# Performance work log

Measured on AMD Instinct MI355X. Metric: run time of the kernel, lower is better.

Reference implementation:

```python
import jax, jax.numpy as jnp
import numpy as np
import math

# Zero-indexed Fano plane lines: {i, i+1, i+3} mod 7
FANO_LINES = np.array([[0,1,3],[1,2,4],[2,3,5],[3,4,6],[4,5,0],[5,6,1],[6,0,2]])
WINDOW = 16  # local window hardcoded in create_expanded_mask

HIDDEN = 896
HEADS = 7
HEAD_DIM = HIDDEN // HEADS  # 128
B, T = 4, 2048


def fano_expanded_mask(T, causal):
    # line membership per head: [7, T] -> True where (j % 7) in line
    jm = np.arange(T) % 7
    line_hit = np.zeros((7, T), dtype=bool)
    for h in range(7):
        line_hit[h] = np.isin(jm, FANO_LINES[h])
    line_hit = jnp.asarray(line_hit)
    i = jnp.arange(T)[:, None]
    j = jnp.arange(T)[None, :]
    if causal:
        causal_m = j <= i                      # [T, T]
        local = (j >= i - WINDOW) & (j <= i)   # causal local window [i-16, i]
        mask = (line_hit[:, None, :] & causal_m[None]) | local[None]
    else:
        local = (j >= i - WINDOW) & (j <= i + WINDOW)
        mask = line_hit[:, None, :] | local[None]
    return mask  # [7, T, T], True = attend


def setup_inputs() -> dict:
    key = jax.random.key(0)
    kx, kq, kk, kv, ko = jax.random.split(key, 5)
    s = 1.0 / math.sqrt(HIDDEN)
    return {
        "x": jax.random.normal(kx, (B, T, HIDDEN), dtype=jnp.float32),
        "Wq": jax.random.normal(kq, (HEADS, HIDDEN, HEAD_DIM), dtype=jnp.float32) * s,
        "Wk": jax.random.normal(kk, (HEADS, HIDDEN, HEAD_DIM), dtype=jnp.float32) * s,
        "Wv": jax.random.normal(kv, (HEADS, HIDDEN, HEAD_DIM), dtype=jnp.float32) * s,
        "Wo": jax.random.normal(ko, (HIDDEN, HIDDEN), dtype=jnp.float32) * s,
        "is_causal": 1,
    }


def reference(x, Wq, Wk, Wv, Wo, is_causal):
    Bx, Tx, H = x.shape
    d = Wq.shape[-1]
    scale = 1.0 / math.sqrt(d)
    # per-head projections (no bias): [7, B, T, d]
    q = jnp.einsum('bth,nhd->nbtd', x, Wq)
    k = jnp.einsum('bth,nhd->nbtd', x, Wk)
    v = jnp.einsum('bth,nhd->nbtd', x, Wv)
    mask = fano_expanded_mask(Tx, bool(is_causal))        # [7, T, T]
    attn = jnp.einsum('nbtd,nbsd->nbts', q, k) * scale    # [7, B, T, T]
    attn = jnp.where(mask[:, None], attn, -jnp.inf)
    attn = jax.nn.softmax(attn, axis=-1)                  # every row has j=i valid
    out = jnp.einsum('nbts,nbsd->nbtd', attn, v)          # [7, B, T, d]
    combined = out.transpose(1, 2, 0, 3).reshape(Bx, Tx, H)  # concat heads
    return combined @ Wo.T
```

## Files before the change

### kernel.cpp

```cpp
#include <hip/hip_runtime.h>
#include <hip/hip_bf16.h>

#define HIDDEN 896
#define HEADS 7
#define HDIM 128
#define BB 4
#define TT 2048
#define MTOT (BB*TT)

#define KSP 132
#define VSP 68
#define PSP 68

#define SCP 896

typedef short bf16x8 __attribute__((ext_vector_type(8)));
typedef float f32x4 __attribute__((ext_vector_type(4)));

__device__ __forceinline__ short f2bf(float f) {
    union { float f; unsigned u; } v; v.f = f;
    unsigned r = (v.u + 0x7FFF + ((v.u >> 16) & 1)) >> 16;
    return (short)r;
}

__device__ __forceinline__ void gll16(const short* g, short* l) {
    __builtin_amdgcn_global_load_lds(
        (const __attribute__((address_space(1))) unsigned int*)g,
        (__attribute__((address_space(3))) unsigned int*)l, 16, 0, 0);
}

__device__ __forceinline__ unsigned linemask(int h) {
    return ((0x0Bu << h) | (0x0Bu >> (7 - h))) & 0x7Fu;
}
__device__ __forceinline__ int linecnt(unsigned m, int X) {
    return (X / 7) * 3 + __popc(m & ((1u << (X % 7)) - 1u));
}

#define NB_CASTX (MTOT * HIDDEN / 1024)
#define NB_CASTWO (HIDDEN * HIDDEN / 1024)
#define NB_TRANS (28 * 4 * 21)
__global__ __launch_bounds__(256) void prep_fused(
    const float* __restrict__ x, const float* __restrict__ Wo,
    const float* __restrict__ Wq, const float* __restrict__ Wk,
    const float* __restrict__ Wv,
    short* __restrict__ xb, short* __restrict__ Wob, short* __restrict__ Wt)
{
    __shared__ float tile[32][33];
    const int bid = blockIdx.x;
    if (bid < NB_CASTX) {
        int base = (bid * 256 + threadIdx.x) * 4;
        float4 v = *(const float4*)(x + base);
        short4 o;
        o.x = f2bf(v.x); o.y = f2bf(v.y); o.z = f2bf(v.z); o.w = f2bf(v.w);
        *(short4*)(xb + base) = o;
    } else if (bid < NB_CASTX + NB_CASTWO) {
        int base = ((bid - NB_CASTX) * 256 + threadIdx.x) * 4;
        float4 v = *(const float4*)(Wo + base);
        short4 o;
        o.x = f2bf(v.x); o.y = f2bf(v.y); o.z = f2bf(v.z); o.w = f2bf(v.w);
        *(short4*)(Wob + base) = o;
    } else {
        int t = bid - NB_CASTX - NB_CASTWO;
        const int z = t / 112;
        const int rem = t % 112;
        const int bx = rem % 28, by = rem / 28;
        const int type = z / 7, head = z % 7;
        const float* src = (type == 0 ? Wq : (type == 1 ? Wk : Wv)) + head * (HIDDEN * HDIM);
        short* dst = Wt + (size_t)z * (HDIM * HIDDEN);
        const int r0 = bx * 32, c0 = by * 32;
        const int tx = threadIdx.x & 31, ty = threadIdx.x >> 5;
        for (int i = 0; i < 4; i++)
            tile[ty * 4 + i][tx] = src[(r0 + ty * 4 + i) * HDIM + c0 + tx];
        __syncthreads();
        for (int i = 0; i < 4; i++)
            dst[(c0 + ty * 4 + i) * HIDDEN + r0 + tx] = f2bf(tile[tx][ty * 4 + i]);
    }
}

__global__ __launch_bounds__(256) void qkv_gemm(
    const short* __restrict__ xb, const short* __restrict__ Wt,
    short* __restrict__ Q, short* __restrict__ Kk, short* __restrict__ Vt)
{
    __shared__ short Ash[3 * 128 * 32];
    __shared__ short Bsh[3 * 128 * 32];
    const int orig = blockIdx.x;
    const int sblk = (orig & 7) * 168 + (orig >> 3);
    const int z = sblk % 21;
    const int m0 = (sblk / 21) * 128;
    const int head = z % 7, type = z / 7;
    const short* Wz = Wt + (size_t)z * (HDIM * HIDDEN);

    const int tid = threadIdx.x;
    const int wave = tid >> 6, lane = tid & 63;
    const int quad = lane >> 4, l16 = lane & 15;
    const int wm = (wave >> 1) * 64, wn = (wave & 1) * 64;

    f32x4 acc[4][4] = {};

    const int r0 = tid >> 2, cc0 = (tid & 3) * 8;
    const int r1 = r0 + 64;
    const short* asrc0 = xb + (size_t)(m0 + r0) * HIDDEN + cc0;
    const short* asrc1 = xb + (size_t)(m0 + r1) * HIDDEN + cc0;
    const short* bsrc0 = Wz + (size_t)r0 * HIDDEN + cc0;
    const short* bsrc1 = Wz + (size_t)r1 * HIDDEN + cc0;

    auto STAGE = [&](int kt, int sel) {
        const int ko = kt * 32;
        short* ab = Ash + sel * 4096;
        short* bb = Bsh + sel * 4096;
        gll16(asrc0 + ko, ab + wave * 512);
        gll16(asrc1 + ko, ab + 2048 + wave * 512);
        gll16(bsrc0 + ko, bb + wave * 512);
        gll16(bsrc1 + ko, bb + 2048 + wave * 512);
    };

    STAGE(0, 0);
    const int NT = HIDDEN / 32;
    for (int t = 0; t < NT; t++) {
        const int sel = t % 3;
        if (t + 1 < NT) {
            STAGE(t + 1, (t + 1) % 3);
            asm volatile("s_waitcnt vmcnt(4)" ::: "memory");
        } else {
            asm volatile("s_waitcnt vmcnt(0)" ::: "memory");
        }
        __builtin_amdgcn_s_barrier();
        __builtin_amdgcn_sched_barrier(0);
        const short* ab = Ash + sel * 4096;
        const short* bb = Bsh + sel * 4096;
        bf16x8 af[4], bfr[4];
        for (int mi = 0; mi < 4; mi++)
            af[mi] = *(const bf16x8*)(ab + (wm + mi * 16 + l16) * 32 + quad * 8);
        for (int ni = 0; ni < 4; ni++)
            bfr[ni] = *(const bf16x8*)(bb + (wn + ni * 16 + l16) * 32 + quad * 8);
        for (int mi = 0; mi < 4; mi++)
            for (int ni = 0; ni < 4; ni++)
                acc[mi][ni] = __builtin_amdgcn_mfma_f32_16x16x32_bf16(af[mi], bfr[ni], acc[mi][ni], 0, 0, 0);
    }

    const size_t base = (size_t)head * (MTOT * HDIM);
    if (type == 0) {
        const float qs = 0.08838834764831845f * 1.4426950408889634f;
        for (int mi = 0; mi < 4; mi++)
            for (int ni = 0; ni < 4; ni++)
                for (int r = 0; r < 4; r++) {
                    int m = m0 + wm + mi * 16 + quad * 4 + r;
                    int n = wn + ni * 16 + l16;
                    Q[base + (size_t)m * HDIM + n] = f2bf(acc[mi][ni][r] * qs);
                }
    } else if (type == 1) {
        for (int mi = 0; mi < 4; mi++)
            for (int ni = 0; ni < 4; ni++)
                for (int r = 0; r < 4; r++) {
                    int m = m0 + wm + mi * 16 + quad * 4 + r;
                    int n = wn + ni * 16 + l16;
                    Kk[base + (size_t)m * HDIM + n] = f2bf(acc[mi][ni][r]);
                }
    } else {
        for (int mi = 0; mi < 4; mi++)
            for (int ni = 0; ni < 4; ni++) {
                int m = m0 + wm + mi * 16 + quad * 4;
                int bb2 = m >> 11, t = m & 2047;
                int n = wn + ni * 16 + l16;
                short4 o;
                o.x = f2bf(acc[mi][ni][0]); o.y = f2bf(acc[mi][ni][1]);
                o.z = f2bf(acc[mi][ni][2]); o.w = f2bf(acc[mi][ni][3]);
                *(short4*)(Vt + base + (size_t)bb2 * (HDIM * TT) + (size_t)n * TT + t) = o;
            }
    }
}

__global__ __launch_bounds__(256) void compact_k(const short* __restrict__ K,
                                                 short* __restrict__ Kc)
{
    const int hb = blockIdx.x, h = hb >> 2, b = hb & 3;
    const unsigned m = linemask(h);
    const int c_tot = 876 + __popc(m & 0xFu);
    const int o0 = __ffs(m) - 1;
    const unsigned m1 = m & (m - 1);
    const int o1 = __ffs(m1) - 1;
    const unsigned m2 = m1 & (m1 - 1);
    const int o2 = __ffs(m2) - 1;
    const int r = blockIdx.y * 32 + (threadIdx.x >> 3);
    const int c = (threadIdx.x & 7) * 16;
    short* dst = Kc + ((size_t)hb * SCP + r) * HDIM + c;
    if (r < c_tot) {
        int g = r / 3, id = r - g * 3;
        int s = g * 7 + (id == 0 ? o0 : (id == 1 ? o1 : o2));
        const short* src = K + (size_t)(h * MTOT + b * TT + s) * HDIM + c;
        *(bf16x8*)dst = *(const bf16x8*)src;
        *(bf16x8*)(dst + 8) = *(const bf16x8*)(src + 8);
    } else {
        bf16x8 zz = {};
        *(bf16x8*)dst = zz;
        *(bf16x8*)(dst + 8) = zz;
    }
}

__global__ __launch_bounds__(256) void compact_v(const short* __restrict__ Vt,
                                                 short* __restrict__ Vc)
{
    const int hb = blockIdx.x, h = hb >> 2, b = hb & 3;
    const int d = blockIdx.y;
    const unsigned m = linemask(h);
    const int c_tot = 876 + __popc(m & 0xFu);
    const int o0 = __ffs(m) - 1;
    const unsigned m1 = m & (m - 1);
    const int o1 = __ffs(m1) - 1;
    const unsigned m2 = m1 & (m1 - 1);
    const int o2 = __ffs(m2) - 1;
    const short* src = Vt + (size_t)h * MTOT * HDIM + (size_t)b * HDIM * TT + (size_t)d * TT;
    short* dst = Vc + ((size_t)hb * HDIM + d) * SCP;
    for (int sp = threadIdx.x * 4; sp < SCP; sp += 1024) {
        short4 o;
        short* po = (short*)&o;
        for (int j = 0; j < 4; j++) {
            int spp = sp + j;
            short v = 0;
            if (spp < c_tot) {
                int g = spp / 3, id = spp - g * 3;
                int s = g * 7 + (id == 0 ? o0 : (id == 1 ? o1 : o2));
                v = src[s];
            }
            po[j] = v;
        }
        *(short4*)(dst + sp) = o;
    }
}

__global__ __launch_bounds__(256) void fano_attn(
    const short* __restrict__ Q, const short* __restrict__ K, const short* __restrict__ Vt,
    const short* __restrict__ Kc, const short* __restrict__ Vc,
    short* __restrict__ Ocat, const int* __restrict__ iscp)
{
    __shared__ short Ks[64 * KSP];
    __shared__ short Vs[128 * VSP];
    __shared__ short Ps[4][32 * PSP];

    const int causal = *iscp;
    const int mlin = blockIdx.y + 4 * blockIdx.z;
    const int qt = (causal && mlin >= 16) ? ((int)gridDim.x - 1 - blockIdx.x)
                                          : (int)blockIdx.x;
    const int q0 = qt * 128;
    const int b = blockIdx.y, h = blockIdx.z;
    const int hb = h * 4 + b;
    const int tid = threadIdx.x, wave = tid >> 6, lane = tid & 63;
    const int quad = lane >> 4, l16 = lane & 15;
    const int iw = q0 + wave * 32;

    const short* Qb = Q + (size_t)(h * MTOT + b * TT + q0) * HDIM;
    const short* Kb = K + (size_t)(h * MTOT + b * TT) * HDIM;
    const short* Vb = Vt + (size_t)h * MTOT * HDIM + (size_t)b * HDIM * TT;
    const short* Kcb = Kc + (size_t)hb * SCP * HDIM;
    const short* Vcb = Vc + (size_t)hb * HDIM * SCP;

    bf16x8 qf[2][4];
    for (int g = 0; g < 2; g++)
        for (int ks = 0; ks < 4; ks++)
            qf[g][ks] = *(const bf16x8*)(Qb + (size_t)(wave * 32 + g * 16 + l16) * HDIM + ks * 32 + quad * 8);

    f32x4 oacc[2][8] = {};
    f32x4 lacc[2] = {};
    int irow[2][4];
    for (int g = 0; g < 2; g++)
        for (int r = 0; r < 4; r++)
            irow[g][r] = q0 + wave * 32 + g * 16 + quad * 4 + r;

    const bf16x8 vones = {0x3F80, 0x3F80, 0x3F80, 0x3F80, 0x3F80, 0x3F80, 0x3F80, 0x3F80};

    int krow[4], kcol[4], vrow[4], vcol[4];
    for (int i = 0; i < 4; i++) {
        int c = tid + i * 256;
        krow[i] = c >> 4; kcol[i] = (c & 15) * 8;
        vrow[i] = c >> 3; vcol[i] = (c & 7) * 8;
    }

    const unsigned m_h = linemask(h);
    const int c_tot = 876 + __popc(m_h & 0xFu);
    const int sB0 = (causal && q0 >= 64) ? (q0 - 64) : 0;
    const int sB1 = causal ? (q0 + 128) : (q0 + 192 < TT ? q0 + 192 : TT);
    const int cA = linecnt(m_h, sB0);
    const int cC0 = causal ? c_tot : linecnt(m_h, sB1);
    const int l16h = (l16 - h + 7) % 7;

    short* Pw = &Ps[wave][0];

    const int nph = causal ? 2 : 3;
    for (int p = 0; p < nph; p++) {
        const short *Kp, *Vp;
        int vstr, t0, t1, c0v = 0, c1v = 0;
        if (p == 0)      { Kp = Kcb; Vp = Vcb; vstr = SCP; t0 = 0;        t1 = (cA + 63) >> 6;    c0v = 0;   c1v = cA; }
        else if (p == 1) { Kp = Kb;  Vp = Vb;  vstr = TT;  t0 = sB0 >> 6; t1 = sB1 >> 6; }
        else             { Kp = Kcb; Vp = Vcb; vstr = SCP; t0 = cC0 >> 6; t1 = (c_tot + 63) >> 6; c0v = cC0; c1v = c_tot; }
        if (t0 >= t1) continue;
        const bool comp = (p != 1);
        int s0q = sB0 % 7;

        bf16x8 kreg[4], vreg[4];
        {
            const int si = t0 * 64;
            for (int i = 0; i < 4; i++) {
                kreg[i] = *(const bf16x8*)(Kp + (size_t)(si + krow[i]) * HDIM + kcol[i]);
                vreg[i] = *(const bf16x8*)(Vp + (size_t)vrow[i] * vstr + si + vcol[i]);
            }
        }

        for (int t = t0; t < t1; t++) {
            const int s0 = t * 64;
            __syncthreads();
            for (int i = 0; i < 4; i++) {
                *(bf16x8*)(Ks + krow[i] * KSP + kcol[i]) = kreg[i];
                *(bf16x8*)(Vs + vrow[i] * VSP + vcol[i]) = vreg[i];
            }
            __syncthreads();

            int tn = t + 1; if (tn >= t1) tn = t0;
            const int sn = tn * 64;
            for (int i = 0; i < 4; i++) {
                kreg[i] = *(const bf16x8*)(Kp + (size_t)(sn + krow[i]) * HDIM + kcol[i]);
                vreg[i] = *(const bf16x8*)(Vp + (size_t)vrow[i] * vstr + sn + vcol[i]);
            }

            f32x4 sacc[2][4] = {};
            for (int ni = 0; ni < 4; ni++)
                for (int ks = 0; ks < 4; ks++) {
                    bf16x8 bk = *(const bf16x8*)(Ks + (ni * 16 + l16) * KSP + ks * 32 + quad * 8);
                    sacc[0][ni] = __builtin_amdgcn_mfma_f32_16x16x32_bf16(qf[0][ks], bk, sacc[0][ni], 0, 0, 0);
                    sacc[1][ni] = __builtin_amdgcn_mfma_f32_16x16x32_bf16(qf[1][ks], bk, sacc[1][ni], 0, 0, 0);
                }

            if (comp) {
                for (int ni = 0; ni < 4; ni++) {
                    int scol = s0 + ni * 16 + l16;
                    bool ok = (scol >= c0v) & (scol < c1v);
                    for (int g = 0; g < 2; g++)
                        for (int r = 0; r < 4; r++)
                            sacc[g][ni][r] = ok ? exp2f(sacc[g][ni][r]) : 0.0f;
                }
            } else {
                int d7b = l16h + s0q; if (d7b >= 7) d7b -= 7;
                for (int ni = 0; ni < 4; ni++) {
                    int d7 = d7b + 2 * ni; if (d7 >= 7) d7 -= 7;
                    bool line = (0x0B >> d7) & 1;
                    int s = s0 + ni * 16 + l16;
                    for (int g = 0; g < 2; g++)
                        for (int r = 0; r < 4; r++) {
                            int i = irow[g][r];
                            bool ok = causal ? ((s <= i) & (line | (s >= i - 16)))
                                             : (line | ((s >= i - 16) & (s <= i + 16)));
                            sacc[g][ni][r] = ok ? exp2f(sacc[g][ni][r]) : 0.0f;
                        }
                }
                s0q++; if (s0q == 7) s0q = 0;
            }

            for (int g = 0; g < 2; g++)
                for (int ni = 0; ni < 4; ni++)
                    for (int r = 0; r < 4; r++)
                        Pw[(g * 16 + quad * 4 + r) * PSP + ni * 16 + l16] = f2bf(sacc[g][ni][r]);

            for (int ks2 = 0; ks2 < 2; ks2++) {
                bf16x8 ap0 = *(const bf16x8*)(Pw + l16 * PSP + ks2 * 32 + quad * 8);
                bf16x8 ap1 = *(const bf16x8*)(Pw + (16 + l16) * PSP + ks2 * 32 + quad * 8);
                lacc[0] = __builtin_amdgcn_mfma_f32_16x16x32_bf16(ap0, vones, lacc[0], 0, 0, 0);
                lacc[1] = __builtin_amdgcn_mfma_f32_16x16x32_bf16(ap1, vones, lacc[1], 0, 0, 0);
                for (int nj = 0; nj < 8; nj++) {
                    bf16x8 bv = *(const bf16x8*)(Vs + (nj * 16 + l16) * VSP + ks2 * 32 + quad * 8);
                    oacc[0][nj] = __builtin_amdgcn_mfma_f32_16x16x32_bf16(ap0, bv, oacc[0][nj], 0, 0, 0);
                    oacc[1][nj] = __builtin_amdgcn_mfma_f32_16x16x32_bf16(ap1, bv, oacc[1][nj], 0, 0, 0);
                }
            }
        }
    }

    short* Obase = Ocat + (size_t)(b * TT) * HIDDEN + h * HDIM;
    for (int g = 0; g < 2; g++) {
        float inv[4];
        for (int r = 0; r < 4; r++) inv[r] = 1.0f / lacc[g][r];
        for (int nj = 0; nj < 8; nj++)
            for (int r = 0; r < 4; r++)
                Obase[(size_t)irow[g][r] * HIDDEN + nj * 16 + l16] = f2bf(oacc[g][nj][r] * inv[r]);
    }
}

__global__ __launch_bounds__(256) void out_gemm(
    const short* __restrict__ A, const short* __restrict__ Bt, float* __restrict__ out)
{
    __shared__ short Ash[3 * 128 * 32];
    __shared__ short Bsh[3 * 128 * 32];
    const int orig = blockIdx.x;
    const int sblk = (orig & 7) * 56 + (orig >> 3);
    const int n0 = (sblk % 7) * 128;
    const int m0 = (sblk / 7) * 128;

    const int tid = threadIdx.x;
    const int wave = tid >> 6, lane = tid & 63;
    const int quad = lane >> 4, l16 = lane & 15;
    const int wm = (wave >> 1) * 64, wn = (wave & 1) * 64;

    f32x4 acc[4][4] = {};

    const int r0 = tid >> 2, cc0 = (tid & 3) * 8;
    const int r1 = r0 + 64;
    const short* asrc0 = A + (size_t)(m0 + r0) * HIDDEN + cc0;
    const short* asrc1 = A + (size_t)(m0 + r1) * HIDDEN + cc0;
    const short* bsrc0 = Bt + (size_t)(n0 + r0) * HIDDEN + cc0;
    const short* bsrc1 = Bt + (size_t)(n0 + r1) * HIDDEN + cc0;

    auto STAGE = [&](int kt, int sel) {
        const int ko = kt * 32;
        short* ab = Ash + sel * 4096;
        short* bb = Bsh + sel * 4096;
        gll16(asrc0 + ko, ab + wave * 512);
        gll16(asrc1 + ko, ab + 2048 + wave * 512);
        gll16(bsrc0 + ko, bb + wave * 512);
        gll16(bsrc1 + ko, bb + 2048 + wave * 512);
    };

    STAGE(0, 0);
    const int NT = HIDDEN / 32;
    for (int t = 0; t < NT; t++) {
        const int sel = t % 3;
        if (t + 1 < NT) {
            STAGE(t + 1, (t + 1) % 3);
            asm volatile("s_waitcnt vmcnt(4)" ::: "memory");
        } else {
            asm volatile("s_waitcnt vmcnt(0)" ::: "memory");
        }
        __builtin_amdgcn_s_barrier();
        __builtin_amdgcn_sched_barrier(0);
        const short* ab = Ash + sel * 4096;
        const short* bb = Bsh + sel * 4096;
        bf16x8 af[4], bfr[4];
        for (int mi = 0; mi < 4; mi++)
            af[mi] = *(const bf16x8*)(ab + (wm + mi * 16 + l16) * 32 + quad * 8);
        for (int ni = 0; ni < 4; ni++)
            bfr[ni] = *(const bf16x8*)(bb + (wn + ni * 16 + l16) * 32 + quad * 8);
        for (int mi = 0; mi < 4; mi++)
            for (int ni = 0; ni < 4; ni++)
                acc[mi][ni] = __builtin_amdgcn_mfma_f32_16x16x32_bf16(af[mi], bfr[ni], acc[mi][ni], 0, 0, 0);
    }

    for (int mi = 0; mi < 4; mi++)
        for (int ni = 0; ni < 4; ni++)
            for (int r = 0; r < 4; r++) {
                int m = m0 + wm + mi * 16 + quad * 4 + r;
                int n = n0 + wn + ni * 16 + l16;
                out[(size_t)m * HIDDEN + n] = acc[mi][ni][r];
            }
}

extern "C" void kernel_launch(void* const* d_in, const int* in_sizes, int n_in,
                              void* d_out, int out_size, void* d_ws, size_t ws_size,
                              hipStream_t stream) {
    (void)in_sizes; (void)n_in; (void)out_size; (void)ws_size;
    const float* x  = (const float*)d_in[0];
    const float* Wq = (const float*)d_in[1];
    const float* Wk = (const float*)d_in[2];
    const float* Wv = (const float*)d_in[3];
    const float* Wo = (const float*)d_in[4];
    const int* iscp = (const int*)d_in[5];
    float* out = (float*)d_out;

    short* xb   = (short*)d_ws;
    short* Qb   = xb   + (size_t)MTOT * HIDDEN;
    short* Kb   = Qb   + (size_t)HEADS * MTOT * HDIM;
    short* Vtb  = Kb   + (size_t)HEADS * MTOT * HDIM;
    short* Ocat = Vtb  + (size_t)HEADS * MTOT * HDIM;
    short* Wt   = Ocat;
    short* Wob  = Ocat + (size_t)MTOT * HIDDEN;
    short* Kc   = xb;
    short* Vc   = Kc + (size_t)28 * SCP * HDIM;

    prep_fused<<<NB_CASTX + NB_CASTWO + NB_TRANS, 256, 0, stream>>>(
        x, Wo, Wq, Wk, Wv, xb, Wob, Wt);
    qkv_gemm<<<21 * (MTOT / 128), 256, 0, stream>>>(xb, Wt, Qb, Kb, Vtb);
    compact_k<<<dim3(28, SCP / 32), 256, 0, stream>>>(Kb, Kc);
    compact_v<<<dim3(28, HDIM), 256, 0, stream>>>(Vtb, Vc);
    fano_attn<<<dim3(TT / 128, BB, HEADS), 256, 0, stream>>>(Qb, Kb, Vtb, Kc, Vc, Ocat, iscp);
    out_gemm<<<(HIDDEN / 128) * (MTOT / 128), 256, 0, stream>>>(Ocat, Wob, out);
}
```

Before: 282.1 us.

## Double-buffer K/V tiles via direct global-to-LDS loads with XOR swizzle in attention

Replaces register-staged K/V tile loads and the padded LDS layout with a double-buffered LDS scheme filled by global_load_lds, prefetching the next tile (even across phases) while computing the current one, with one barrier per tile. LDS layouts for K, V and P switch from padding to XOR swizzling to avoid bank conflicts. The band-phase mask is simplified for tiles far from the diagonal, where only the Fano line test applies. Shared memory use roughly doubles, which may reduce occupancy.

```diff
diff --git a/kernel.cpp b/kernel.cpp
--- a/kernel.cpp
+++ b/kernel.cpp
@@ -7,10 +7,6 @@
 #define BB 4
 #define TT 2048
 #define MTOT (BB*TT)
-
-#define KSP 132
-#define VSP 68
-#define PSP 68
 
 #define SCP 896
 
@@ -233,9 +229,9 @@
     const short* __restrict__ Kc, const short* __restrict__ Vc,
     short* __restrict__ Ocat, const int* __restrict__ iscp)
 {
-    __shared__ short Ks[64 * KSP];
-    __shared__ short Vs[128 * VSP];
-    __shared__ short Ps[4][32 * PSP];
+    __shared__ short Ks[2 * 64 * 128];
+    __shared__ short Vs[2 * 128 * 64];
+    __shared__ short Ps[4 * 2048];
 
     const int causal = *iscp;
     const int mlin = blockIdx.y + 4 * blockIdx.z;
@@ -247,12 +243,29 @@
     const int tid = threadIdx.x, wave = tid >> 6, lane = tid & 63;
     const int quad = lane >> 4, l16 = lane & 15;
     const int iw = q0 + wave * 32;
+    const int swz = l16 & 7;
 
     const short* Qb = Q + (size_t)(h * MTOT + b * TT + q0) * HDIM;
     const short* Kb = K + (size_t)(h * MTOT + b * TT) * HDIM;
     const short* Vb = Vt + (size_t)h * MTOT * HDIM + (size_t)b * HDIM * TT;
     const short* Kcb = Kc + (size_t)hb * SCP * HDIM;
     const short* Vcb = Vc + (size_t)hb * HDIM * SCP;
+
+    int krowS[4], kccS[4], vrowS[4], vccS[4];
+    for (int i = 0; i < 4; i++) {
+        int c = (wave * 4 + i) * 64 + lane;
+        krowS[i] = c >> 4; kccS[i] = ((c & 15) ^ (krowS[i] & 7)) * 8;
+        vrowS[i] = c >> 3; vccS[i] = ((c & 7) ^ (vrowS[i] & 7)) * 8;
+    }
+
+    auto STAGE = [&](const short* Kp, const short* Vp, int vstr, int s0, int sel) {
+        short* kb = Ks + sel * 8192;
+        short* vb = Vs + sel * 8192;
+        for (int i = 0; i < 4; i++) {
+            gll16(Kp + (size_t)(s0 + krowS[i]) * HDIM + kccS[i], kb + (wave * 4 + i) * 512);
+            gll16(Vp + (size_t)vrowS[i] * vstr + s0 + vccS[i], vb + (wave * 4 + i) * 512);
+        }
+    };
 
     bf16x8 qf[2][4];
     for (int g = 0; g < 2; g++)
@@ -267,13 +280,6 @@
             irow[g][r] = q0 + wave * 32 + g * 16 + quad * 4 + r;
 
     const bf16x8 vones = {0x3F80, 0x3F80, 0x3F80, 0x3F80, 0x3F80, 0x3F80, 0x3F80, 0x3F80};
-
-    int krow[4], kcol[4], vrow[4], vcol[4];
-    for (int i = 0; i < 4; i++) {
-        int c = tid + i * 256;
-        krow[i] = c >> 4; kcol[i] = (c & 15) * 8;
-        vrow[i] = c >> 3; vcol[i] = (c & 7) * 8;
-    }
 
     const unsigned m_h = linemask(h);
     const int c_tot = 876 + __popc(m_h & 0xFu);
@@ -283,48 +289,48 @@
     const int cC0 = causal ? c_tot : linecnt(m_h, sB1);
     const int l16h = (l16 - h + 7) % 7;
 
-    short* Pw = &Ps[wave][0];
-
-    const int nph = causal ? 2 : 3;
-    for (int p = 0; p < nph; p++) {
-        const short *Kp, *Vp;
-        int vstr, t0, t1, c0v = 0, c1v = 0;
-        if (p == 0)      { Kp = Kcb; Vp = Vcb; vstr = SCP; t0 = 0;        t1 = (cA + 63) >> 6;    c0v = 0;   c1v = cA; }
-        else if (p == 1) { Kp = Kb;  Vp = Vb;  vstr = TT;  t0 = sB0 >> 6; t1 = sB1 >> 6; }
-        else             { Kp = Kcb; Vp = Vcb; vstr = SCP; t0 = cC0 >> 6; t1 = (c_tot + 63) >> 6; c0v = cC0; c1v = c_tot; }
-        if (t0 >= t1) continue;
-        const bool comp = (p != 1);
-        int s0q = sB0 % 7;
-
-        bf16x8 kreg[4], vreg[4];
-        {
-            const int si = t0 * 64;
-            for (int i = 0; i < 4; i++) {
-                kreg[i] = *(const bf16x8*)(Kp + (size_t)(si + krow[i]) * HDIM + kcol[i]);
-                vreg[i] = *(const bf16x8*)(Vp + (size_t)vrow[i] * vstr + si + vcol[i]);
-            }
-        }
-
-        for (int t = t0; t < t1; t++) {
+    const short* Kpa[3]; const short* Vpa[3];
+    int vstra[3], ta0[3], ta1[3], cv0a[3], cv1a[3], cmpa[3];
+    int np = 0;
+    {
+        int t1A = (cA + 63) >> 6;
+        if (t1A > 0) { Kpa[np] = Kcb; Vpa[np] = Vcb; vstra[np] = SCP; ta0[np] = 0; ta1[np] = t1A; cv0a[np] = 0; cv1a[np] = cA; cmpa[np] = 1; np++; }
+    }
+    {
+        int t0B = sB0 >> 6, t1B = sB1 >> 6;
+        if (t1B > t0B) { Kpa[np] = Kb; Vpa[np] = Vb; vstra[np] = TT; ta0[np] = t0B; ta1[np] = t1B; cv0a[np] = 0; cv1a[np] = 0; cmpa[np] = 0; np++; }
+    }
+    if (!causal) {
+        int t0C = cC0 >> 6, t1C = (c_tot + 63) >> 6;
+        if (t1C > t0C) { Kpa[np] = Kcb; Vpa[np] = Vcb; vstra[np] = SCP; ta0[np] = t0C; ta1[np] = t1C; cv0a[np] = cC0; cv1a[np] = c_tot; cmpa[np] = 1; np++; }
+    }
+
+    short* Pw = Ps + wave * 2048;
+    int cur = 0;
+    STAGE(Kpa[0], Vpa[0], vstra[0], ta0[0] * 64, 0);
+
+    for (int pi = 0; pi < np; pi++) {
+        const short* Kp_ = Kpa[pi];
+        const short* Vp_ = Vpa[pi];
+        const int vstr_ = vstra[pi], t1_ = ta1[pi];
+        const int comp = cmpa[pi], c0v = cv0a[pi], c1v = cv1a[pi];
+        for (int t = ta0[pi]; t < t1_; t++) {
+            asm volatile("s_waitcnt vmcnt(0)" ::: "memory");
+            __builtin_amdgcn_s_barrier();
+            __builtin_amdgcn_sched_barrier(0);
+            if (t + 1 < t1_)
+                STAGE(Kp_, Vp_, vstr_, (t + 1) * 64, cur ^ 1);
+            else if (pi + 1 < np)
+                STAGE(Kpa[pi + 1], Vpa[pi + 1], vstra[pi + 1], ta0[pi + 1] * 64, cur ^ 1);
+
+            const short* KsC = Ks + cur * 8192;
+            const short* VsC = Vs + cur * 8192;
             const int s0 = t * 64;
-            __syncthreads();
-            for (int i = 0; i < 4; i++) {
-                *(bf16x8*)(Ks + krow[i] * KSP + kcol[i]) = kreg[i];
-                *(bf16x8*)(Vs + vrow[i] * VSP + vcol[i]) = vreg[i];
-            }
-            __syncthreads();
-
-            int tn = t + 1; if (tn >= t1) tn = t0;
-            const int sn = tn * 64;
-            for (int i = 0; i < 4; i++) {
-                kreg[i] = *(const bf16x8*)(Kp + (size_t)(sn + krow[i]) * HDIM + kcol[i]);
-                vreg[i] = *(const bf16x8*)(Vp + (size_t)vrow[i] * vstr + sn + vcol[i]);
-            }
 
             f32x4 sacc[2][4] = {};
             for (int ni = 0; ni < 4; ni++)
                 for (int ks = 0; ks < 4; ks++) {
-                    bf16x8 bk = *(const bf16x8*)(Ks + (ni * 16 + l16) * KSP + ks * 32 + quad * 8);
+                    bf16x8 bk = *(const bf16x8*)(KsC + (ni * 16 + l16) * 128 + ((ks * 4 + quad) ^ swz) * 8);
                     sacc[0][ni] = __builtin_amdgcn_mfma_f32_16x16x32_bf16(qf[0][ks], bk, sacc[0][ni], 0, 0, 0);
                     sacc[1][ni] = __builtin_amdgcn_mfma_f32_16x16x32_bf16(qf[1][ks], bk, sacc[1][ni], 0, 0, 0);
                 }
@@ -338,38 +344,52 @@
                             sacc[g][ni][r] = ok ? exp2f(sacc[g][ni][r]) : 0.0f;
                 }
             } else {
-                int d7b = l16h + s0q; if (d7b >= 7) d7b -= 7;
-                for (int ni = 0; ni < 4; ni++) {
-                    int d7 = d7b + 2 * ni; if (d7 >= 7) d7 -= 7;
-                    bool line = (0x0B >> d7) & 1;
-                    int s = s0 + ni * 16 + l16;
-                    for (int g = 0; g < 2; g++)
-                        for (int r = 0; r < 4; r++) {
-                            int i = irow[g][r];
-                            bool ok = causal ? ((s <= i) & (line | (s >= i - 16)))
-                                             : (line | ((s >= i - 16) & (s <= i + 16)));
-                            sacc[g][ni][r] = ok ? exp2f(sacc[g][ni][r]) : 0.0f;
-                        }
+                const bool full = (s0 + 80 > iw) && (causal || (s0 < iw + 48));
+                int d7b = l16h + (t % 7); if (d7b >= 7) d7b -= 7;
+                if (full) {
+                    for (int ni = 0; ni < 4; ni++) {
+                        int d7 = d7b + 2 * ni; if (d7 >= 7) d7 -= 7;
+                        bool line = (0x0B >> d7) & 1;
+                        int s = s0 + ni * 16 + l16;
+                        for (int g = 0; g < 2; g++)
+                            for (int r = 0; r < 4; r++) {
+                                int i = irow[g][r];
+                                bool ok = causal ? ((s <= i) & (line | (s >= i - 16)))
+                                                 : (line | ((s >= i - 16) & (s <= i + 16)));
+                                sacc[g][ni][r] = ok ? exp2f(sacc[g][ni][r]) : 0.0f;
+                            }
+                    }
+                } else {
+                    for (int ni = 0; ni < 4; ni++) {
+                        int d7 = d7b + 2 * ni; if (d7 >= 7) d7 -= 7;
+                        bool line = (0x0B >> d7) & 1;
+                        for (int g = 0; g < 2; g++)
+                            for (int r = 0; r < 4; r++)
+                                sacc[g][ni][r] = line ? exp2f(sacc[g][ni][r]) : 0.0f;
+                    }
                 }
-                s0q++; if (s0q == 7) s0q = 0;
             }
 
             for (int g = 0; g < 2; g++)
                 for (int ni = 0; ni < 4; ni++)
-                    for (int r = 0; r < 4; r++)
-                        Pw[(g * 16 + quad * 4 + r) * PSP + ni * 16 + l16] = f2bf(sacc[g][ni][r]);
+                    for (int r = 0; r < 4; r++) {
+                        int row = g * 16 + quad * 4 + r;
+                        Pw[row * 64 + (((ni * 2 + (l16 >> 3)) ^ (row & 7)) * 8) + (l16 & 7)]
+                            = f2bf(sacc[g][ni][r]);
+                    }
 
             for (int ks2 = 0; ks2 < 2; ks2++) {
-                bf16x8 ap0 = *(const bf16x8*)(Pw + l16 * PSP + ks2 * 32 + quad * 8);
-                bf16x8 ap1 = *(const bf16x8*)(Pw + (16 + l16) * PSP + ks2 * 32 + quad * 8);
+                bf16x8 ap0 = *(const bf16x8*)(Pw + l16 * 64 + ((ks2 * 4 + quad) ^ swz) * 8);
+                bf16x8 ap1 = *(const bf16x8*)(Pw + (16 + l16) * 64 + ((ks2 * 4 + quad) ^ swz) * 8);
                 lacc[0] = __builtin_amdgcn_mfma_f32_16x16x32_bf16(ap0, vones, lacc[0], 0, 0, 0);
                 lacc[1] = __builtin_amdgcn_mfma_f32_16x16x32_bf16(ap1, vones, lacc[1], 0, 0, 0);
                 for (int nj = 0; nj < 8; nj++) {
-                    bf16x8 bv = *(const bf16x8*)(Vs + (nj * 16 + l16) * VSP + ks2 * 32 + quad * 8);
+                    bf16x8 bv = *(const bf16x8*)(VsC + (nj * 16 + l16) * 64 + ((ks2 * 4 + quad) ^ swz) * 8);
                     oacc[0][nj] = __builtin_amdgcn_mfma_f32_16x16x32_bf16(ap0, bv, oacc[0][nj], 0, 0, 0);
                     oacc[1][nj] = __builtin_amdgcn_mfma_f32_16x16x32_bf16(ap1, bv, oacc[1][nj], 0, 0, 0);
                 }
             }
+            cur ^= 1;
         }
     }
 
```

Result: no change. 279.6 us (-0.9%).
